# Kernel optimization log

Hardware: AMD Instinct MI355X
Metric: run time of the kernel (lower is better)

The kernel has to match this reference:

```python
import jax, jax.numpy as jnp
import numpy as np

B, V, T, C, DIM, HID, OUT = 8192, 101, 30, 4, 64, 128, 1

def setup_inputs() -> dict:
    key = jax.random.key(0)
    ks = jax.random.split(key, 20)
    stdv = 1.0 / np.sqrt(V)
    def lin(k, fan_in, fan_out):
        k1, k2 = jax.random.split(k)
        bound = 1.0 / np.sqrt(fan_in)
        W = jax.random.uniform(k1, (fan_in, fan_out), jnp.float32, -bound, bound)
        b = jax.random.uniform(k2, (fan_out,), jnp.float32, -bound, bound)
        return W, b
    W1, b1 = lin(ks[1], C, DIM)
    W2, b2 = lin(ks[2], DIM, DIM)
    Wz, bz = lin(ks[3], C + 2 * DIM, DIM)
    Wr, br = lin(ks[4], C + 2 * DIM, DIM)
    Ww, bw = lin(ks[5], C + 2 * DIM, DIM)
    Wf1, bf1 = lin(ks[6], DIM * V, HID)
    Wf2, bf2 = lin(ks[7], HID, OUT * V)
    return {
        'x': jax.random.normal(ks[0], (B, V, T, C), jnp.float32),
        'dyn': jax.random.uniform(ks[8], (V, V), jnp.float32, -stdv, stdv),
        'W1': W1, 'b1': b1, 'W2': W2, 'b2': b2,
        'Wz': Wz, 'bz': bz, 'Wr': Wr, 'br': br, 'Ww': Ww, 'bw': bw,
        'Wf1': Wf1, 'bf1': bf1, 'Wf2': Wf2, 'bf2': bf2,
    }

def reference(x, dyn, W1, b1, W2, b2, Wz, bz, Wr, br, Ww, bw, Wf1, bf1, Wf2, bf2):
    b = x.shape[0]
    # (B, V, T, C) -> (T, B, V, C) for scan over time
    xs = jnp.transpose(x, (2, 0, 1, 3))
    h0 = jnp.zeros((b, V, DIM), x.dtype)

    def step(h, xt):
        # two-layer graph diffusion conv: dyn @ feat, then Linear+tanh
        f = jnp.tanh(jnp.einsum('uv,bvc->buc', dyn, xt) @ W1 + b1)   # (b,V,64)
        f = jnp.tanh(jnp.einsum('uv,bvd->bud', dyn, f) @ W2 + b2)    # (b,V,64)
        cat = jnp.concatenate([xt, f, h], axis=-1)                   # (b,V,132)
        z = jax.nn.sigmoid(cat @ Wz + bz)
        r = jax.nn.sigmoid(cat @ Wr + br)
        cat2 = jnp.concatenate([xt, f, r * h], axis=-1)
        cn = jnp.tanh(cat2 @ Ww + bw)
        h_new = (1.0 - z) * h + z * cn
        return h_new, None

    ht, _ = jax.lax.scan(step, h0, xs)
    flat = ht.reshape(b, V * DIM)
    out = jax.nn.relu(flat @ Wf1 + bf1) @ Wf2 + bf2                  # (b, V)
    return jax.nn.softmax(out, axis=-1)
```

## Files before the change

### kernel.cpp

```cpp
#include <hip/hip_runtime.h>
#include <cmath>

#define B_    8192
#define V_    101
#define T_    30
#define C_    4
#define D_    64
#define HID_  128

typedef __attribute__((ext_vector_type(8))) short  short8;
typedef __attribute__((ext_vector_type(4))) float  f32x4;

#define MFMA16(a, b, c) __builtin_amdgcn_mfma_f32_16x16x32_bf16((a), (b), (c), 0, 0, 0)

#define WZT_OFF   0
#define WRT_OFF   10752
#define WWT_OFF   21504
#define CA_OFF    32256
#define GRH_OFF   53760
#define F1T_OFF   62976
#define XBT_OFF   71680
#define YF_USH    76032
#define LDS_USH   77312
#define YFF       (YF_USH/2)

__device__ __forceinline__ unsigned short f2b(float f) {
    unsigned u = __float_as_uint(f);
    u += 0x7fffu + ((u >> 16) & 1u);
    return (unsigned short)(u >> 16);
}
__device__ __forceinline__ float b2f(unsigned short h) {
    return __uint_as_float(((unsigned)h) << 16);
}
__device__ __forceinline__ float fast_tanh(float x) {
    float s = __builtin_amdgcn_exp2f(2.885390081777926817f * x);
    return 1.f - 2.f * __builtin_amdgcn_rcpf(s + 1.f);
}
__device__ __forceinline__ float fast_sigmoid(float x) {
    return __builtin_amdgcn_rcpf(1.f + __builtin_amdgcn_exp2f(-1.4426950408889634f * x));
}
__device__ __forceinline__ unsigned pk_bf16(float lo, float hi) {
    unsigned r;
    asm("v_cvt_pk_bf16_f32 %0, %1, %2" : "=v"(r) : "v"(lo), "v"(hi));
    return r;
}
__device__ __forceinline__ void st2_bf16(unsigned short* p0, unsigned short* p1, float a, float b) {
    unsigned pk = pk_bf16(a, b);
    *p0 = (unsigned short)pk;
    *p1 = (unsigned short)(pk >> 16);
}
#define FENCE() do { asm volatile("s_waitcnt lgkmcnt(0)" ::: "memory"); \
                     __builtin_amdgcn_sched_barrier(0); } while (0)

__global__ void build_images(const float* __restrict__ dyn,
                             const float* __restrict__ Wz, const float* __restrict__ Wr,
                             const float* __restrict__ Ww, const float* __restrict__ W2,
                             unsigned short* __restrict__ dimg,
                             unsigned short* __restrict__ zimg,
                             unsigned short* __restrict__ rimg,
                             unsigned short* __restrict__ wimg,
                             unsigned short* __restrict__ w2img)
{
    int tid = blockIdx.x * blockDim.x + threadIdx.x;
    int nth = gridDim.x * blockDim.x;
    for (int i = tid; i < 128 * 136; i += nth) {
        int u = i / 136, v = i - u * 136;
        dimg[i] = (u < V_ && v < V_) ? f2b(dyn[u * V_ + v]) : (unsigned short)0;
    }
    for (int i = tid; i < 64 * 168; i += nth) {
        int n = i / 168, k = i - n * 168;
        unsigned short vz = 0, vr = 0, vw = 0;
        if (k < 132) {
            int gk = (k < 128) ? (k + 4) : (k - 128);
            vz = f2b(Wz[gk * 64 + n]);
            vr = f2b(Wr[gk * 64 + n]);
            vw = f2b(Ww[gk * 64 + n]);
        }
        zimg[i] = vz; rimg[i] = vr; wimg[i] = vw;
    }
    for (int i = tid; i < 64 * 72; i += nth) {
        int n = i / 72, k = i - n * 72;
        w2img[i] = (k < 64) ? f2b(W2[k * 64 + n]) : (unsigned short)0;
    }
}

__global__ void __launch_bounds__(512, 2)
mgcgru_mfma(const float* __restrict__ x,
            const unsigned short* __restrict__ dimg,
            const unsigned short* __restrict__ zimg,
            const unsigned short* __restrict__ rimg,
            const unsigned short* __restrict__ wimg,
            const unsigned short* __restrict__ w2img,
            const float* __restrict__ W1, const float* __restrict__ b1,
            const float* __restrict__ b2, const float* __restrict__ bz,
            const float* __restrict__ br, const float* __restrict__ bw,
            const float* __restrict__ Wf1, const float* __restrict__ bf1,
            const float* __restrict__ Wf2, const float* __restrict__ bf2,
            unsigned short* __restrict__ wsflat,
            float* __restrict__ out, int mode)
{
    extern __shared__ unsigned short sm[];
    float* smf = (float*)sm;
    const int tid  = threadIdx.x;
    const int b    = blockIdx.x;
    const int wv   = tid >> 6;
    const int lane = tid & 63;
    const int l16  = lane & 15;
    const int quad = lane >> 4;
    const int mt   = wv;

    {
        unsigned* p = (unsigned*)sm;
        for (int i = tid; i < LDS_USH / 2; i += 512) p[i] = 0u;
    }
    __syncthreads();
    for (int i = tid; i < 1344; i += 512) {
        ((uint4*)&sm[WZT_OFF])[i] = ((const uint4*)zimg)[i];
        ((uint4*)&sm[WRT_OFF])[i] = ((const uint4*)rimg)[i];
        ((uint4*)&sm[WWT_OFF])[i] = ((const uint4*)wimg)[i];
    }

    short8 dynf[4];
    #pragma unroll
    for (int kt = 0; kt < 4; ++kt)
        dynf[kt] = *(const short8*)(dimg + (mt * 16 + l16) * 136 + kt * 32 + quad * 8);
    short8 w2f[4][2];
    #pragma unroll
    for (int nt = 0; nt < 4; ++nt)
        #pragma unroll
        for (int kt = 0; kt < 2; ++kt)
            w2f[nt][kt] = *(const short8*)(w2img + (nt * 16 + l16) * 72 + kt * 32 + quad * 8);
    float w1r[4][4], b1r[4];
    #pragma unroll
    for (int c = 0; c < 4; ++c)
        #pragma unroll
        for (int k = 0; k < 4; ++k)
            w1r[c][k] = W1[c * 64 + l16 + 16 * k];
    #pragma unroll
    for (int k = 0; k < 4; ++k) b1r[k] = b1[l16 + 16 * k];
    float b2r[4], bzr[4], brr[4], bwr[4];
    #pragma unroll
    for (int nt = 0; nt < 4; ++nt) {
        int cc = nt * 16 + l16;
        b2r[nt] = b2[cc]; bzr[nt] = bz[cc]; brr[nt] = br[cc]; bwr[nt] = bw[cc];
    }

    float hreg[4][4] = {{0.f,0.f,0.f,0.f},{0.f,0.f,0.f,0.f},{0.f,0.f,0.f,0.f},{0.f,0.f,0.f,0.f}};
    float zreg[4][4];

    const float* xb = x + (size_t)b * (V_ * T_ * C_);
    const int  xv  = mt * 16 + (lane >> 2);
    const int  xc  = lane & 3;
    const bool xok = (xv < V_);

    {
        float x0 = xok ? xb[xv * (T_ * C_) + xc] : 0.f;
        if (xok) {
            unsigned short h16 = f2b(x0);
            sm[XBT_OFF + xc * 136 + xv]     = h16;
            sm[CA_OFF + xv * 168 + 128 + xc] = h16;
        }
    }
    __syncthreads();

    float xnf = 0.f;
    for (int t = 0; t < T_; ++t) {
        const int sCur  = t & 1;
        const int sNext = sCur ^ 1;
        if (t < T_ - 1 && xok) xnf = xb[xv * (T_ * C_) + (t + 1) * C_ + xc];

        {
            f32x4 accy = {0.f, 0.f, 0.f, 0.f};
            #pragma unroll
            for (int kt = 0; kt < 4; ++kt) {
                short8 bb = *(const short8*)&sm[XBT_OFF + sCur * 2176 + l16 * 136 + kt * 32 + quad * 8];
                accy = MFMA16(dynf[kt], bb, accy);
            }
            if (l16 < 4) {
                #pragma unroll
                for (int e = 0; e < 4; ++e)
                    smf[YFF + (mt * 16 + quad * 4 + e) * 5 + l16] = accy[e];
            }
        }
        FENCE();

        {
            float yv[4][4];
            #pragma unroll
            for (int e = 0; e < 4; ++e)
                #pragma unroll
                for (int c = 0; c < 4; ++c)
                    yv[e][c] = smf[YFF + (mt * 16 + quad * 4 + e) * 5 + c];
            #pragma unroll
            for (int k = 0; k < 4; ++k) {
                float fe[4];
                #pragma unroll
                for (int e = 0; e < 4; ++e)
                    fe[e] = fast_tanh(b1r[k] + yv[e][0] * w1r[0][k] + yv[e][1] * w1r[1][k]
                                              + yv[e][2] * w1r[2][k] + yv[e][3] * w1r[3][k]);
                uint2 uv;
                uv.x = pk_bf16(fe[0], fe[1]);
                uv.y = pk_bf16(fe[2], fe[3]);
                *(uint2*)&sm[F1T_OFF + (l16 + 16 * k) * 136 + mt * 16 + quad * 4] = uv;
            }
        }
        if (t < T_ - 1 && xok) {
            unsigned short h16 = f2b(xnf);
            sm[XBT_OFF + sNext * 2176 + xc * 136 + xv]      = h16;
            sm[CA_OFF + xv * 168 + 128 + 8 * sNext + xc]    = h16;
        }
        __syncthreads();

        {
            f32x4 ag[4] = {{0.f,0.f,0.f,0.f},{0.f,0.f,0.f,0.f},{0.f,0.f,0.f,0.f},{0.f,0.f,0.f,0.f}};
            #pragma unroll
            for (int kt = 0; kt < 4; ++kt) {
                #pragma unroll
                for (int nt = 0; nt < 4; ++nt) {
                    short8 bb = *(const short8*)&sm[F1T_OFF + (nt * 16 + l16) * 136 + kt * 32 + quad * 8];
                    ag[nt] = MFMA16(dynf[kt], bb, ag[nt]);
                }
            }
            #pragma unroll
            for (int nt = 0; nt < 4; nt += 2)
                #pragma unroll
                for (int e = 0; e < 4; ++e) {
                    int row = mt * 16 + quad * 4 + e;
                    st2_bf16(&sm[GRH_OFF + row * 72 + nt * 16 + l16],
                             &sm[GRH_OFF + row * 72 + (nt + 1) * 16 + l16],
                             ag[nt][e], ag[nt + 1][e]);
                }
        }
        FENCE();

        {
            f32x4 af[4] = {{0.f,0.f,0.f,0.f},{0.f,0.f,0.f,0.f},{0.f,0.f,0.f,0.f},{0.f,0.f,0.f,0.f}};
            #pragma unroll
            for (int kt = 0; kt < 2; ++kt) {
                short8 a = *(const short8*)&sm[GRH_OFF + (mt * 16 + l16) * 72 + kt * 32 + quad * 8];
                #pragma unroll
                for (int nt = 0; nt < 4; ++nt)
                    af[nt] = MFMA16(a, w2f[nt][kt], af[nt]);
            }
            #pragma unroll
            for (int nt = 0; nt < 4; nt += 2)
                #pragma unroll
                for (int e = 0; e < 4; ++e) {
                    int row = mt * 16 + quad * 4 + e;
                    st2_bf16(&sm[CA_OFF + row * 168 + nt * 16 + l16],
                             &sm[CA_OFF + row * 168 + (nt + 1) * 16 + l16],
                             fast_tanh(af[nt][e] + b2r[nt]),
                             fast_tanh(af[nt + 1][e] + b2r[nt + 1]));
                }
        }
        FENCE();

        {
            f32x4 az[4] = {{0.f,0.f,0.f,0.f},{0.f,0.f,0.f,0.f},{0.f,0.f,0.f,0.f},{0.f,0.f,0.f,0.f}};
            f32x4 ar[4] = {{0.f,0.f,0.f,0.f},{0.f,0.f,0.f,0.f},{0.f,0.f,0.f,0.f},{0.f,0.f,0.f,0.f}};
            #pragma unroll
            for (int kt = 0; kt < 5; ++kt) {
                short8 a;
                if (kt < 4)
                    a = *(const short8*)&sm[CA_OFF + (mt * 16 + l16) * 168 + kt * 32 + quad * 8];
                else
                    a = *(const short8*)&sm[CA_OFF + (mt * 16 + l16) * 168 + 128 + 8 * sCur + quad * 8];
                #pragma unroll
                for (int nt = 0; nt < 4; ++nt) {
                    short8 bzf = *(const short8*)&sm[WZT_OFF + (nt * 16 + l16) * 168 + kt * 32 + quad * 8];
                    short8 brf = *(const short8*)&sm[WRT_OFF + (nt * 16 + l16) * 168 + kt * 32 + quad * 8];
                    az[nt] = MFMA16(a, bzf, az[nt]);
                    ar[nt] = MFMA16(a, brf, ar[nt]);
                }
            }
            #pragma unroll
            for (int nt = 0; nt < 4; nt += 2)
                #pragma unroll
                for (int e = 0; e < 4; ++e) {
                    int row = mt * 16 + quad * 4 + e;
                    zreg[nt][e]     = fast_sigmoid(az[nt][e] + bzr[nt]);
                    zreg[nt + 1][e] = fast_sigmoid(az[nt + 1][e] + bzr[nt + 1]);
                    float r0 = fast_sigmoid(ar[nt][e] + brr[nt]);
                    float r1 = fast_sigmoid(ar[nt + 1][e] + brr[nt + 1]);
                    st2_bf16(&sm[GRH_OFF + row * 72 + nt * 16 + l16],
                             &sm[GRH_OFF + row * 72 + (nt + 1) * 16 + l16],
                             r0 * hreg[nt][e], r1 * hreg[nt + 1][e]);
                }
        }
        FENCE();

        {
            f32x4 ac[4] = {{0.f,0.f,0.f,0.f},{0.f,0.f,0.f,0.f},{0.f,0.f,0.f,0.f},{0.f,0.f,0.f,0.f}};
            #pragma unroll
            for (int kt = 0; kt < 5; ++kt) {
                short8 a;
                if (kt < 2)
                    a = *(const short8*)&sm[CA_OFF + (mt * 16 + l16) * 168 + kt * 32 + quad * 8];
                else if (kt < 4)
                    a = *(const short8*)&sm[GRH_OFF + (mt * 16 + l16) * 72 + (kt - 2) * 32 + quad * 8];
                else
                    a = *(const short8*)&sm[CA_OFF + (mt * 16 + l16) * 168 + 128 + 8 * sCur + quad * 8];
                #pragma unroll
                for (int nt = 0; nt < 4; ++nt) {
                    short8 bwf = *(const short8*)&sm[WWT_OFF + (nt * 16 + l16) * 168 + kt * 32 + quad * 8];
                    ac[nt] = MFMA16(a, bwf, ac[nt]);
                }
            }
            #pragma unroll
            for (int nt = 0; nt < 4; nt += 2)
                #pragma unroll
                for (int e = 0; e < 4; ++e) {
                    int row = mt * 16 + quad * 4 + e;
                    float cn0 = fast_tanh(ac[nt][e] + bwr[nt]);
                    float cn1 = fast_tanh(ac[nt + 1][e] + bwr[nt + 1]);
                    float h0 = hreg[nt][e]     + zreg[nt][e]     * (cn0 - hreg[nt][e]);
                    float h1 = hreg[nt + 1][e] + zreg[nt + 1][e] * (cn1 - hreg[nt + 1][e]);
                    hreg[nt][e] = h0; hreg[nt + 1][e] = h1;
                    st2_bf16(&sm[CA_OFF + row * 168 + 64 + nt * 16 + l16],
                             &sm[CA_OFF + row * 168 + 64 + (nt + 1) * 16 + l16],
                             h0, h1);
                }
        }
    }

    __syncthreads();

    if (mode == 1) {
        for (int i = tid; i < 808; i += 512) {
            int v = i >> 3, d8 = (i & 7) * 8;
            *(uint4*)(wsflat + (size_t)b * 6464 + v * 64 + d8) =
                *(const uint4*)&sm[CA_OFF + v * 168 + 64 + d8];
        }
    } else {
        {
            int j = tid & 127, part = tid >> 7;
            float acc = 0.f;
            int k0 = part * 1616;
            for (int k = k0; k < k0 + 1616; ++k) {
                int v = k >> 6, d = k & 63;
                acc += b2f(sm[CA_OFF + v * 168 + 64 + d]) * Wf1[(size_t)k * 128 + j];
            }
            smf[part * 128 + j] = acc;
        }
        __syncthreads();
        if (tid < 128) {
            float s = bf1[tid];
            for (int p = 0; p < 4; ++p) s += smf[p * 128 + tid];
            smf[512 + tid] = fmaxf(s, 0.f);
        }
        __syncthreads();
        for (int i = tid; i < 128 * 101; i += 512) smf[1024 + i] = Wf2[i];
        __syncthreads();
        if (tid < V_) {
            float s = bf2[tid];
            for (int j = 0; j < 128; ++j) s += smf[512 + j] * smf[1024 + j * 101 + tid];
            smf[14000 + tid] = s;
        }
        __syncthreads();
        if (tid < V_) {
            float m = -1e30f;
            for (int u = 0; u < V_; ++u) m = fmaxf(m, smf[14000 + u]);
            smf[14110 + tid] = expf(smf[14000 + tid] - m);
        }
        __syncthreads();
        if (tid < V_) {
            float s = 0.f;
            for (int u = 0; u < V_; ++u) s += smf[14110 + u];
            out[(size_t)b * V_ + tid] = smf[14110 + tid] / s;
        }
    }
}

__global__ void __launch_bounds__(256)
head1_gemm(const unsigned short* __restrict__ flat,
           const float* __restrict__ Wf1,
           const float* __restrict__ bf1,
           float* __restrict__ A1)
{
    __shared__ __align__(16) unsigned short AT[32 * 40 + 128 * 40];
    unsigned short* BT = AT + 32 * 40;
    const int tid  = threadIdx.x;
    const int Mb   = blockIdx.x * 32;
    const int wv   = tid >> 6, lane = tid & 63;
    const int l16  = lane & 15, quad = lane >> 4;
    const int mt   = wv & 1;
    const int ntB  = (wv >> 1) * 4;
    f32x4 acc[4] = {{0.f,0.f,0.f,0.f},{0.f,0.f,0.f,0.f},{0.f,0.f,0.f,0.f},{0.f,0.f,0.f,0.f}};

    for (int kt = 0; kt < 202; ++kt) {
        uint4 av;
        if (tid < 128) {
            int row = tid >> 2, k8 = (tid & 3) * 8;
            av = *(const uint4*)(flat + (size_t)(Mb + row) * 6464 + kt * 32 + k8);
        }
        float4 bv[4];
        #pragma unroll
        for (int p = 0; p < 4; ++p) {
            int g = tid + p * 256, k = g >> 5, nq = g & 31;
            bv[p] = *(const float4*)&Wf1[(size_t)(kt * 32 + k) * 128 + nq * 4];
        }
        __syncthreads();
        if (tid < 128) {
            int row = tid >> 2, k8 = (tid & 3) * 8;
            *(uint4*)&AT[row * 40 + k8] = av;
        }
        #pragma unroll
        for (int p = 0; p < 4; ++p) {
            int g = tid + p * 256, k = g >> 5, nq = g & 31;
            BT[(nq*4 + 0) * 40 + k] = f2b(bv[p].x);
            BT[(nq*4 + 1) * 40 + k] = f2b(bv[p].y);
            BT[(nq*4 + 2) * 40 + k] = f2b(bv[p].z);
            BT[(nq*4 + 3) * 40 + k] = f2b(bv[p].w);
        }
        __syncthreads();
        short8 a = *(const short8*)&AT[(mt*16 + l16) * 40 + quad * 8];
        #pragma unroll
        for (int i = 0; i < 4; ++i) {
            short8 bb = *(const short8*)&BT[((ntB + i)*16 + l16) * 40 + quad * 8];
            acc[i] = MFMA16(a, bb, acc[i]);
        }
    }
    #pragma unroll
    for (int i = 0; i < 4; ++i)
        #pragma unroll
        for (int e = 0; e < 4; ++e) {
            int row = Mb + mt*16 + quad*4 + e;
            int col = (ntB + i)*16 + l16;
            A1[(size_t)row * 128 + col] = fmaxf(acc[i][e] + bf1[col], 0.f);
        }
}

__global__ void head2_softmax(const float* __restrict__ A1,
                              const float* __restrict__ Wf2,
                              const float* __restrict__ bf2,
                              float* __restrict__ out)
{
    extern __shared__ float s3[];
    float* WF = s3;
    float* AR = s3 + 12928;
    float* LG = AR + 128;
    float* EG = LG + 104;
    const int tid = threadIdx.x;
    for (int i = tid; i < 128 * 101; i += 128) WF[i] = Wf2[i];
    for (int r = 0; r < 64; ++r) {
        size_t row = (size_t)blockIdx.x * 64 + r;
        __syncthreads();
        AR[tid] = A1[row * 128 + tid];
        __syncthreads();
        if (tid < V_) {
            float s = bf2[tid];
            for (int j = 0; j < 128; ++j) s += AR[j] * WF[j * 101 + tid];
            LG[tid] = s;
        }
        __syncthreads();
        if (tid < V_) {
            float m = -1e30f;
            for (int u = 0; u < V_; ++u) m = fmaxf(m, LG[u]);
            EG[tid] = expf(LG[tid] - m);
        }
        __syncthreads();
        if (tid < V_) {
            float s = 0.f;
            for (int u = 0; u < V_; ++u) s += EG[u];
            out[row * 101 + tid] = EG[tid] / s;
        }
    }
}

extern "C" void kernel_launch(void* const* d_in, const int* in_sizes, int n_in,
                              void* d_out, int out_size, void* d_ws, size_t ws_size,
                              hipStream_t stream) {
    const float* x   = (const float*)d_in[0];
    const float* dyn = (const float*)d_in[1];
    const float* W1  = (const float*)d_in[2];
    const float* b1  = (const float*)d_in[3];
    const float* W2  = (const float*)d_in[4];
    const float* b2  = (const float*)d_in[5];
    const float* Wz  = (const float*)d_in[6];
    const float* bz  = (const float*)d_in[7];
    const float* Wr  = (const float*)d_in[8];
    const float* br  = (const float*)d_in[9];
    const float* Ww  = (const float*)d_in[10];
    const float* bw  = (const float*)d_in[11];
    const float* Wf1 = (const float*)d_in[12];
    const float* bf1 = (const float*)d_in[13];
    const float* Wf2 = (const float*)d_in[14];
    const float* bf2 = (const float*)d_in[15];
    float* out = (float*)d_out;

    const size_t FLAT_B = (size_t)B_ * 6464 * 2;
    const size_t A1_B   = (size_t)B_ * 128 * 4;
    const size_t IMG_B  = (size_t)(17408 + 3 * 10752 + 4608) * 2;
    int mode = (ws_size >= FLAT_B + A1_B + IMG_B) ? 1 : 0;

    char* wsc = (char*)d_ws;
    unsigned short* wsflat = nullptr;
    float* A1p = nullptr;
    unsigned short* img;
    if (mode) {
        wsflat = (unsigned short*)wsc;
        A1p    = (float*)(wsc + FLAT_B);
        img    = (unsigned short*)(wsc + FLAT_B + A1_B);
    } else {
        img    = (unsigned short*)wsc;
    }
    unsigned short* dimg  = img;
    unsigned short* zimg  = dimg + 17408;
    unsigned short* rimg  = zimg + 10752;
    unsigned short* wimg  = rimg + 10752;
    unsigned short* w2img = wimg + 10752;

    build_images<<<64, 256, 0, stream>>>(dyn, Wz, Wr, Ww, W2,
                                         dimg, zimg, rimg, wimg, w2img);

    (void)hipFuncSetAttribute((const void*)mgcgru_mfma,
                              hipFuncAttributeMaxDynamicSharedMemorySize, LDS_USH * 2);
    mgcgru_mfma<<<B_, 512, LDS_USH * 2, stream>>>(
        x, dimg, zimg, rimg, wimg, w2img,
        W1, b1, b2, bz, br, bw, Wf1, bf1, Wf2, bf2, wsflat, out, mode);

    if (mode) {
        head1_gemm<<<B_ / 32, 256, 0, stream>>>(wsflat, Wf1, bf1, A1p);
        head2_softmax<<<B_ / 64, 128, (12928 + 128 + 104 + 104) * 4, stream>>>(A1p, Wf2, bf2, out);
    }
}
```

Before: 5.932 ms.

## Keep candidate-gate weights in registers, swizzle LDS rows, overlap candidate MFMAs across fence

Moves the Ww weight fragments from LDS into per-wave registers, which shrinks the LDS footprint and removes the LDS reads for the candidate gate. Adds an XOR swizzle on the CA and GRH row indexing to reduce LDS bank conflicts. Splits the candidate GEMM so the x and f parts are computed before the fence and only the r*h part after it, letting that work overlap the barrier. The extra 20 short8 fragments per thread raise register pressure, which may lower occupancy or cause spills.

```diff
diff --git a/kernel.cpp b/kernel.cpp
--- a/kernel.cpp
+++ b/kernel.cpp
@@ -15,14 +15,16 @@
 
 #define WZT_OFF   0
 #define WRT_OFF   10752
-#define WWT_OFF   21504
-#define CA_OFF    32256
-#define GRH_OFF   53760
-#define F1T_OFF   62976
-#define XBT_OFF   71680
-#define YF_USH    76032
-#define LDS_USH   77312
+#define CA_OFF    21504
+#define GRH_OFF   43008
+#define F1T_OFF   52224
+#define XBT_OFF   60928
+#define YF_USH    65280
+#define LDS_USH   66560
 #define YFF       (YF_USH/2)
+
+#define CAi(r,c)  (CA_OFF  + ((((r)*168) + (c)) ^ ((((r)>>3)&1)<<4)))
+#define GRHi(r,c) (GRH_OFF + ((((r)*72)  + (c)) ^ ((((r)>>3)&1)<<4)))
 
 __device__ __forceinline__ unsigned short f2b(float f) {
     unsigned u = __float_as_uint(f);
@@ -117,7 +119,6 @@
     for (int i = tid; i < 1344; i += 512) {
         ((uint4*)&sm[WZT_OFF])[i] = ((const uint4*)zimg)[i];
         ((uint4*)&sm[WRT_OFF])[i] = ((const uint4*)rimg)[i];
-        ((uint4*)&sm[WWT_OFF])[i] = ((const uint4*)wimg)[i];
     }
 
     short8 dynf[4];
@@ -130,6 +131,12 @@
         #pragma unroll
         for (int kt = 0; kt < 2; ++kt)
             w2f[nt][kt] = *(const short8*)(w2img + (nt * 16 + l16) * 72 + kt * 32 + quad * 8);
+    short8 wwf[4][5];
+    #pragma unroll
+    for (int nt = 0; nt < 4; ++nt)
+        #pragma unroll
+        for (int kt = 0; kt < 5; ++kt)
+            wwf[nt][kt] = *(const short8*)(wimg + (nt * 16 + l16) * 168 + kt * 32 + quad * 8);
     float w1r[4][4], b1r[4];
     #pragma unroll
     for (int c = 0; c < 4; ++c)
@@ -157,8 +164,8 @@
         float x0 = xok ? xb[xv * (T_ * C_) + xc] : 0.f;
         if (xok) {
             unsigned short h16 = f2b(x0);
-            sm[XBT_OFF + xc * 136 + xv]     = h16;
-            sm[CA_OFF + xv * 168 + 128 + xc] = h16;
+            sm[XBT_OFF + xc * 136 + xv] = h16;
+            sm[CAi(xv, 128 + xc)]       = h16;
         }
     }
     __syncthreads();
@@ -206,8 +213,8 @@
         }
         if (t < T_ - 1 && xok) {
             unsigned short h16 = f2b(xnf);
-            sm[XBT_OFF + sNext * 2176 + xc * 136 + xv]      = h16;
-            sm[CA_OFF + xv * 168 + 128 + 8 * sNext + xc]    = h16;
+            sm[XBT_OFF + sNext * 2176 + xc * 136 + xv] = h16;
+            sm[CAi(xv, 128 + 8 * sNext + xc)]          = h16;
         }
         __syncthreads();
 
@@ -226,8 +233,8 @@
                 #pragma unroll
                 for (int e = 0; e < 4; ++e) {
                     int row = mt * 16 + quad * 4 + e;
-                    st2_bf16(&sm[GRH_OFF + row * 72 + nt * 16 + l16],
-                             &sm[GRH_OFF + row * 72 + (nt + 1) * 16 + l16],
+                    st2_bf16(&sm[GRHi(row, nt * 16 + l16)],
+                             &sm[GRHi(row, (nt + 1) * 16 + l16)],
                              ag[nt][e], ag[nt + 1][e]);
                 }
         }
@@ -237,7 +244,7 @@
             f32x4 af[4] = {{0.f,0.f,0.f,0.f},{0.f,0.f,0.f,0.f},{0.f,0.f,0.f,0.f},{0.f,0.f,0.f,0.f}};
             #pragma unroll
             for (int kt = 0; kt < 2; ++kt) {
-                short8 a = *(const short8*)&sm[GRH_OFF + (mt * 16 + l16) * 72 + kt * 32 + quad * 8];
+                short8 a = *(const short8*)&sm[GRHi(mt * 16 + l16, kt * 32 + quad * 8)];
                 #pragma unroll
                 for (int nt = 0; nt < 4; ++nt)
                     af[nt] = MFMA16(a, w2f[nt][kt], af[nt]);
@@ -247,8 +254,8 @@
                 #pragma unroll
                 for (int e = 0; e < 4; ++e) {
                     int row = mt * 16 + quad * 4 + e;
-                    st2_bf16(&sm[CA_OFF + row * 168 + nt * 16 + l16],
-                             &sm[CA_OFF + row * 168 + (nt + 1) * 16 + l16],
+                    st2_bf16(&sm[CAi(row, nt * 16 + l16)],
+                             &sm[CAi(row, (nt + 1) * 16 + l16)],
                              fast_tanh(af[nt][e] + b2r[nt]),
                              fast_tanh(af[nt + 1][e] + b2r[nt + 1]));
                 }
@@ -262,9 +269,9 @@
             for (int kt = 0; kt < 5; ++kt) {
                 short8 a;
                 if (kt < 4)
-                    a = *(const short8*)&sm[CA_OFF + (mt * 16 + l16) * 168 + kt * 32 + quad * 8];
+                    a = *(const short8*)&sm[CAi(mt * 16 + l16, kt * 32 + quad * 8)];
                 else
-                    a = *(const short8*)&sm[CA_OFF + (mt * 16 + l16) * 168 + 128 + 8 * sCur + quad * 8];
+                    a = *(const short8*)&sm[CAi(mt * 16 + l16, 128 + 8 * sCur + quad * 8)];
                 #pragma unroll
                 for (int nt = 0; nt < 4; ++nt) {
                     short8 bzf = *(const short8*)&sm[WZT_OFF + (nt * 16 + l16) * 168 + kt * 32 + quad * 8];
@@ -278,33 +285,43 @@
                 #pragma unroll
                 for (int e = 0; e < 4; ++e) {
                     int row = mt * 16 + quad * 4 + e;
-                    zreg[nt][e]     = fast_sigmoid(az[nt][e] + bzr[nt]);
-                    zreg[nt + 1][e] = fast_sigmoid(az[nt + 1][e] + bzr[nt + 1]);
                     float r0 = fast_sigmoid(ar[nt][e] + brr[nt]);
                     float r1 = fast_sigmoid(ar[nt + 1][e] + brr[nt + 1]);
-                    st2_bf16(&sm[GRH_OFF + row * 72 + nt * 16 + l16],
-                             &sm[GRH_OFF + row * 72 + (nt + 1) * 16 + l16],
+                    st2_bf16(&sm[GRHi(row, nt * 16 + l16)],
+                             &sm[GRHi(row, (nt + 1) * 16 + l16)],
                              r0 * hreg[nt][e], r1 * hreg[nt + 1][e]);
                 }
-        }
-        FENCE();
-
-        {
-            f32x4 ac[4] = {{0.f,0.f,0.f,0.f},{0.f,0.f,0.f,0.f},{0.f,0.f,0.f,0.f},{0.f,0.f,0.f,0.f}};
-            #pragma unroll
-            for (int kt = 0; kt < 5; ++kt) {
+            #pragma unroll
+            for (int nt = 0; nt < 4; ++nt)
+                #pragma unroll
+                for (int e = 0; e < 4; ++e)
+                    zreg[nt][e] = fast_sigmoid(az[nt][e] + bzr[nt]);
+        }
+
+        f32x4 ac[4] = {{0.f,0.f,0.f,0.f},{0.f,0.f,0.f,0.f},{0.f,0.f,0.f,0.f},{0.f,0.f,0.f,0.f}};
+        {
+            #pragma unroll
+            for (int kk = 0; kk < 3; ++kk) {
+                const int kt = (kk < 2) ? kk : 4;
                 short8 a;
                 if (kt < 2)
-                    a = *(const short8*)&sm[CA_OFF + (mt * 16 + l16) * 168 + kt * 32 + quad * 8];
-                else if (kt < 4)
-                    a = *(const short8*)&sm[GRH_OFF + (mt * 16 + l16) * 72 + (kt - 2) * 32 + quad * 8];
+                    a = *(const short8*)&sm[CAi(mt * 16 + l16, kt * 32 + quad * 8)];
                 else
-                    a = *(const short8*)&sm[CA_OFF + (mt * 16 + l16) * 168 + 128 + 8 * sCur + quad * 8];
-                #pragma unroll
-                for (int nt = 0; nt < 4; ++nt) {
-                    short8 bwf = *(const short8*)&sm[WWT_OFF + (nt * 16 + l16) * 168 + kt * 32 + quad * 8];
-                    ac[nt] = MFMA16(a, bwf, ac[nt]);
-                }
+                    a = *(const short8*)&sm[CAi(mt * 16 + l16, 128 + 8 * sCur + quad * 8)];
+                #pragma unroll
+                for (int nt = 0; nt < 4; ++nt)
+                    ac[nt] = MFMA16(a, wwf[nt][kt], ac[nt]);
+            }
+        }
+        FENCE();
+
+        {
+            #pragma unroll
+            for (int kt = 2; kt < 4; ++kt) {
+                short8 a = *(const short8*)&sm[GRHi(mt * 16 + l16, (kt - 2) * 32 + quad * 8)];
+                #pragma unroll
+                for (int nt = 0; nt < 4; ++nt)
+                    ac[nt] = MFMA16(a, wwf[nt][kt], ac[nt]);
             }
             #pragma unroll
             for (int nt = 0; nt < 4; nt += 2)
@@ -316,8 +333,8 @@
                     float h0 = hreg[nt][e]     + zreg[nt][e]     * (cn0 - hreg[nt][e]);
                     float h1 = hreg[nt + 1][e] + zreg[nt + 1][e] * (cn1 - hreg[nt + 1][e]);
                     hreg[nt][e] = h0; hreg[nt + 1][e] = h1;
-                    st2_bf16(&sm[CA_OFF + row * 168 + 64 + nt * 16 + l16],
-                             &sm[CA_OFF + row * 168 + 64 + (nt + 1) * 16 + l16],
+                    st2_bf16(&sm[CAi(row, 64 + nt * 16 + l16)],
+                             &sm[CAi(row, 64 + (nt + 1) * 16 + l16)],
                              h0, h1);
                 }
         }
@@ -329,7 +346,7 @@
         for (int i = tid; i < 808; i += 512) {
             int v = i >> 3, d8 = (i & 7) * 8;
             *(uint4*)(wsflat + (size_t)b * 6464 + v * 64 + d8) =
-                *(const uint4*)&sm[CA_OFF + v * 168 + 64 + d8];
+                *(const uint4*)&sm[CAi(v, 64 + d8)];
         }
     } else {
         {
@@ -338,7 +355,7 @@
             int k0 = part * 1616;
             for (int k = k0; k < k0 + 1616; ++k) {
                 int v = k >> 6, d = k & 63;
-                acc += b2f(sm[CA_OFF + v * 168 + 64 + d]) * Wf1[(size_t)k * 128 + j];
+                acc += b2f(sm[CAi(v, 64 + d)]) * Wf1[(size_t)k * 128 + j];
             }
             smf[part * 128 + j] = acc;
         }
```

Result: slower. 10.95 ms (+84.5%).
